# Kernel tuning notes

Hardware: AMD Instinct MI355X
Metric: run time of the kernel (lower is better)

## Reference

```python
import jax, jax.numpy as jnp
import numpy as np

B, NQ, NV = 4, 16384, 16384
DIM, FRAMES = 64, 4
D = DIM * FRAMES            # embed_dims = 256
HEADS, POINTS, LEVELS = 8, 4, 1
HD = D // HEADS             # head_dim = 32
HL, WL = 128, 128           # single-level feature map, HL*WL == NV
EPS = 1e-6


def setup_inputs() -> dict:
    key = jax.random.key(0)
    ks = jax.random.split(key, 14)
    inp = {
        "query": jax.random.normal(ks[0], (B, NQ, D), jnp.float32),
        "feat": jax.random.normal(ks[1], (B, NV, D), jnp.float32),
        "reference_points": jax.random.uniform(ks[2], (B, NQ, LEVELS, 2), jnp.float32),
        "spatial_shapes": jnp.array([[HL, WL]], jnp.int32),
        "level_start_index": jnp.array([0], jnp.int32),
        # LayerNorm params
        "qn_scale": jnp.ones((D,), jnp.float32),
        "qn_bias": jnp.zeros((D,), jnp.float32),
        "fn_scale": jnp.ones((D,), jnp.float32),
        "fn_bias": jnp.zeros((D,), jnp.float32),
        # MSDeformAttn projections
        "W_value": jax.random.normal(ks[3], (D, D), jnp.float32) / np.sqrt(D),
        "b_value": jnp.zeros((D,), jnp.float32),
        "W_off": jax.random.normal(ks[4], (D, HEADS * LEVELS * POINTS * 2), jnp.float32) * 0.01,
        "b_off": jax.random.normal(ks[5], (HEADS * LEVELS * POINTS * 2,), jnp.float32) * 0.5,
        "W_attn": jax.random.normal(ks[6], (D, HEADS * LEVELS * POINTS), jnp.float32) * 0.02,
        "b_attn": jnp.zeros((HEADS * LEVELS * POINTS,), jnp.float32),
        "W_out": jax.random.normal(ks[7], (D, D), jnp.float32) / np.sqrt(D),
        "b_out": jnp.zeros((D,), jnp.float32),
        # gamma is a learned scale (init 0 in the module; randomized here so it contributes)
        "gamma": jax.random.normal(ks[8], (D,), jnp.float32) * 0.1,
    }
    return inp


def _layer_norm(x, scale, bias):
    mu = jnp.mean(x, axis=-1, keepdims=True)
    var = jnp.mean(jnp.square(x - mu), axis=-1, keepdims=True)
    return (x - mu) * jax.lax.rsqrt(var + EPS) * scale + bias


def _bilinear_gather(v, loc, Hl, Wl):
    # v:   [B, H, N, hd] flattened level values (row-major HxW)
    # loc: [B, H, NQ, P, 2] normalized sampling locations in [0,1]
    # grid_sample semantics: align_corners=False, zero padding
    x = loc[..., 0] * Wl - 0.5
    y = loc[..., 1] * Hl - 0.5
    x0 = jnp.floor(x); y0 = jnp.floor(y)
    x1 = x0 + 1.0;     y1 = y0 + 1.0
    wx1 = x - x0; wx0 = 1.0 - wx1
    wy1 = y - y0; wy0 = 1.0 - wy1
    out = 0.0
    for xi, yi, w in ((x0, y0, wx0 * wy0), (x1, y0, wx1 * wy0),
                      (x0, y1, wx0 * wy1), (x1, y1, wx1 * wy1)):
        inb = (xi >= 0) & (xi < Wl) & (yi >= 0) & (yi < Hl)
        idx = (jnp.clip(yi, 0, Hl - 1) * Wl + jnp.clip(xi, 0, Wl - 1)).astype(jnp.int32)
        Bc, Hc, NQc, Pc = idx.shape
        g = jnp.take_along_axis(v, idx.reshape(Bc, Hc, NQc * Pc)[..., None], axis=2)
        g = g.reshape(Bc, Hc, NQc, Pc, -1)          # [B, H, NQ, P, hd]
        out = out + g * (w * inb)[..., None]
    return out


def reference(query, feat, reference_points, spatial_shapes, level_start_index,
              qn_scale, qn_bias, fn_scale, fn_bias,
              W_value, b_value, W_off, b_off, W_attn, b_attn, W_out, b_out, gamma):
    Bq, nq, _ = query.shape
    q = _layer_norm(query, qn_scale, qn_bias)
    v = _layer_norm(feat, fn_scale, fn_bias)

    # value projection -> per-head values [B, H, NV, hd]
    value = (v @ W_value + b_value).reshape(Bq, -1, HEADS, HD).transpose(0, 2, 1, 3)

    # sampling offsets [B, NQ, H, L, P, 2] and attention weights (softmax over L*P)
    off = (q @ W_off + b_off).reshape(Bq, nq, HEADS, LEVELS, POINTS, 2)
    aw = jax.nn.softmax((q @ W_attn + b_attn).reshape(Bq, nq, HEADS, LEVELS * POINTS), axis=-1)
    aw = aw.reshape(Bq, nq, HEADS, LEVELS, POINTS)

    ss = np.asarray(spatial_shapes)          # static level geometry
    lsi = np.asarray(level_start_index)
    offset_norm = ss[:, ::-1].astype(np.float32)  # (W, H) per level
    # sampling locations [B, NQ, H, L, P, 2]
    loc = reference_points[:, :, None, :, None, :] + off / offset_norm[None, None, None, :, None, :]

    acc = jnp.zeros((Bq, HEADS, nq, HD), query.dtype)
    for l in range(LEVELS):
        Hl, Wl = int(ss[l, 0]), int(ss[l, 1])
        start = int(lsi[l])
        v_l = value[:, :, start:start + Hl * Wl]                # [B, H, Hl*Wl, hd]
        loc_l = loc[:, :, :, l].transpose(0, 2, 1, 3, 4)        # [B, H, NQ, P, 2]
        sampled = _bilinear_gather(v_l, loc_l, Hl, Wl)          # [B, H, NQ, P, hd]
        aw_l = aw[:, :, :, l].transpose(0, 2, 1, 3)             # [B, H, NQ, P]
        acc = acc + jnp.einsum('bhnpd,bhnp->bhnd', sampled, aw_l)

    out = acc.transpose(0, 2, 1, 3).reshape(Bq, nq, D) @ W_out + b_out
    return query + gamma * out
```

## Files before the change

### kernel.cpp

```cpp
#include <hip/hip_runtime.h>

#define NQ 16384
#define NV 16384
#define DMODEL 256

typedef __bf16 bf16x8 __attribute__((ext_vector_type(8)));
typedef float f32x4 __attribute__((ext_vector_type(4)));

__device__ __forceinline__ unsigned short f2bf(float x) {
    union { float f; unsigned int u; } v; v.f = x;
    unsigned int r = v.u + 0x7fff + ((v.u >> 16) & 1);
    return (unsigned short)(r >> 16);
}
__device__ __forceinline__ float blo(unsigned int u) {
    union { unsigned int u; float f; } v; v.u = u << 16; return v.f;
}
__device__ __forceinline__ float bhi(unsigned int u) {
    union { unsigned int u; float f; } v; v.u = u & 0xFFFF0000u; return v.f;
}
__device__ __forceinline__ f32x4 mfma16(bf16x8 a, bf16x8 b, f32x4 c) {
    return __builtin_amdgcn_mfma_f32_16x16x32_bf16(a, b, c, 0, 0, 0);
}

__global__ __launch_bounds__(256) void k_prep(
    const float* __restrict__ Wv, const float* __restrict__ Woff,
    const float* __restrict__ Wattn, const float* __restrict__ Wout,
    const float* __restrict__ fns, const float* __restrict__ fnb,
    const float* __restrict__ qns, const float* __restrict__ qnb,
    const float* __restrict__ b_value, const float* __restrict__ b_off,
    const float* __restrict__ b_attn,
    unsigned short* __restrict__ WtV, unsigned short* __restrict__ WtC,
    unsigned short* __restrict__ WtO,
    float* __restrict__ csumV, float* __restrict__ preV,
    float* __restrict__ csumC, float* __restrict__ preC) {
    const int blk = blockIdx.x;
    if (blk < 608) {
        int t = blk * 256 + threadIdx.x;
        if (t < 65536) { int n = t >> 8, k = t & 255; WtV[t] = f2bf(fns[k] * Wv[k * 256 + n]); return; }
        t -= 65536;
        if (t < 65536) { int n = t >> 8, k = t & 255; WtO[t] = f2bf(Wout[k * 256 + n]); return; }
        t -= 65536;
        if (t < 24576) {
            int j = t >> 8, k = t & 255;
            float w = (j < 64) ? Woff[k * 64 + j] : Wattn[k * 32 + (j - 64)];
            WtC[j * 256 + k] = f2bf(qns[k] * w);
        }
        return;
    }
    if (blk < 612) {
        __shared__ float sCS[4][64], sPR[4][64];
        const int nl = threadIdx.x & 63;
        const int n = (blk - 608) * 64 + nl;
        const int kp = threadIdx.x >> 6;
        float cs = 0.f, pr = 0.f;
        for (int k = kp * 64; k < kp * 64 + 64; ++k) {
            float w = Wv[k * 256 + n];
            cs += fns[k] * w;
            pr += fnb[k] * w;
        }
        sCS[kp][nl] = cs; sPR[kp][nl] = pr;
        __syncthreads();
        if (threadIdx.x < 64) {
            int nn = (blk - 608) * 64 + threadIdx.x;
            csumV[nn] = sCS[0][threadIdx.x] + sCS[1][threadIdx.x] + sCS[2][threadIdx.x] + sCS[3][threadIdx.x];
            preV[nn] = sPR[0][threadIdx.x] + sPR[1][threadIdx.x] + sPR[2][threadIdx.x] + sPR[3][threadIdx.x]
                       + b_value[nn];
        }
        return;
    }
    {
        __shared__ float sCS[2][96], sPR[2][96];
        const int t = threadIdx.x;
        if (t < 192) {
            const int n = t % 96;
            const int kp = t / 96;
            float cs = 0.f, pr = 0.f;
            for (int k = kp * 128; k < kp * 128 + 128; ++k) {
                float w = (n < 64) ? Woff[k * 64 + n] : Wattn[k * 32 + (n - 64)];
                cs += qns[k] * w;
                pr += qnb[k] * w;
            }
            sCS[kp][n] = cs; sPR[kp][n] = pr;
        }
        __syncthreads();
        if (t < 96) {
            csumC[t] = sCS[0][t] + sCS[1][t];
            preC[t] = sPR[0][t] + sPR[1][t] + ((t < 64) ? b_off[t] : b_attn[t - 64]);
        }
        return;
    }
}

#define STAGE_LNSTATS64(srcptr)                                                       \
    {                                                                                 \
        const int t = threadIdx.x;                                                    \
        const float4* src4 = (const float4*)((srcptr) + (size_t)m0 * 256);            \
        _Pragma("unroll 4") for (int i = 0; i < 16; ++i) {                            \
            float4 x = src4[i * 256 + t];                                             \
            const int row = i * 4 + (t >> 6);                                         \
            uint2 pk;                                                                 \
            pk.x = (unsigned)f2bf(x.x) | ((unsigned)f2bf(x.y) << 16);                 \
            pk.y = (unsigned)f2bf(x.z) | ((unsigned)f2bf(x.w) << 16);                 \
            *(uint2*)&A[row * 264 + (t & 63) * 4] = pk;                               \
        }                                                                             \
    }                                                                                 \
    __syncthreads();                                                                  \
    {                                                                                 \
        const int t = threadIdx.x;                                                    \
        const int r = t >> 2, h = t & 3;                                              \
        float s = 0.f, sq = 0.f;                                                      \
        _Pragma("unroll") for (int j = 0; j < 8; ++j) {                               \
            uint4 u = *(const uint4*)&A[r * 264 + h * 64 + j * 8];                    \
            float v0 = blo(u.x), v1 = bhi(u.x), v2 = blo(u.y), v3 = bhi(u.y);         \
            float v4 = blo(u.z), v5 = bhi(u.z), v6 = blo(u.w), v7 = bhi(u.w);         \
            s += v0 + v1 + v2 + v3 + v4 + v5 + v6 + v7;                               \
            sq += v0 * v0 + v1 * v1 + v2 * v2 + v3 * v3 +                             \
                  v4 * v4 + v5 * v5 + v6 * v6 + v7 * v7;                              \
        }                                                                             \
        s += __shfl_xor(s, 1);  sq += __shfl_xor(sq, 1);                              \
        s += __shfl_xor(s, 2);  sq += __shfl_xor(sq, 2);                              \
        if (h == 0) {                                                                 \
            float mu = s * 0.00390625f;                                               \
            muL[r] = mu;                                                              \
            rsL[r] = rsqrtf(sq * 0.00390625f - mu * mu + 1e-6f);                      \
        }                                                                             \
    }

#define STAGE_A64(srcbuf)                                                             \
    {                                                                                 \
        const int c = threadIdx.x & 31;                                               \
        const int rt = threadIdx.x >> 5;                                              \
        _Pragma("unroll") for (int i = 0; i < 8; ++i) {                               \
            const int r = rt + i * 8;                                                 \
            *(uint4*)&A[r * 264 + c * 8] =                                            \
                *(const uint4*)((srcbuf) + (size_t)(m0 + r) * 256 + c * 8);           \
        }                                                                             \
    }

#define MFMA_STEP4(bf, kk)                                                            \
    _Pragma("unroll") for (int m = 0; m < 4; ++m) {                                   \
        bf16x8 a = *(const bf16x8*)&A[(m * 16 + lrow) * 264 + (kk) * 32 + lk];        \
        _Pragma("unroll") for (int i = 0; i < 4; ++i)                                 \
            acc[i][m] = mfma16(bf[i], a, acc[i][m]);                                  \
    }

__global__ __launch_bounds__(256, 4) void k_mlp(
    const float* __restrict__ feat, const float* __restrict__ csumV,
    const float* __restrict__ preV, const unsigned short* __restrict__ WtV,
    unsigned short* __restrict__ value,
    const float* __restrict__ query, const float* __restrict__ refpt,
    const float* __restrict__ csumC, const float* __restrict__ preC,
    const unsigned short* __restrict__ WtC, float4* __restrict__ samples) {
    __shared__ unsigned short A[64 * 264];
    __shared__ float muL[64], rsL[64];
    const int blk = blockIdx.x;
    const int m0 = (blk >> 1) * 64;
    const int lane = threadIdx.x & 63;
    const int w = threadIdx.x >> 6;

    if ((blk & 1) == 0) {
        STAGE_LNSTATS64(feat)
        const int lrow = lane & 15, lk = (lane >> 4) * 8;
        f32x4 acc[4][4];
#pragma unroll
        for (int i = 0; i < 4; ++i)
#pragma unroll
            for (int m = 0; m < 4; ++m) acc[i][m] = (f32x4){0.f, 0.f, 0.f, 0.f};
#define LOADB_V(dst, kk)                                                              \
    _Pragma("unroll") for (int i = 0; i < 4; ++i) dst[i] =                            \
        *(const bf16x8*)(WtV + (size_t)((w * 4 + i) * 16 + lrow) * 256 + (kk) * 32 + lk);
        {
            bf16x8 b0[4], b1[4];
            LOADB_V(b0, 0)
#pragma unroll
            for (int k2 = 0; k2 < 4; ++k2) {
                LOADB_V(b1, k2 * 2 + 1)
                MFMA_STEP4(b0, k2 * 2)
                if (k2 < 3) { LOADB_V(b0, k2 * 2 + 2) }
                MFMA_STEP4(b1, k2 * 2 + 1)
            }
        }
        __syncthreads();
        const int g = lane >> 4;
#pragma unroll
        for (int i = 0; i < 4; ++i) {
            const int col0 = (w * 4 + i) * 16 + g * 4;
            float4 cs = *(const float4*)(csumV + col0);
            float4 pr = *(const float4*)(preV + col0);
#pragma unroll
            for (int m = 0; m < 4; ++m) {
                const int rl = m * 16 + (lane & 15);
                float mu = muL[rl], rs = rsL[rl];
                uint2 r;
                r.x = (unsigned)f2bf(rs * (acc[i][m][0] - mu * cs.x) + pr.x) |
                      ((unsigned)f2bf(rs * (acc[i][m][1] - mu * cs.y) + pr.y) << 16);
                r.y = (unsigned)f2bf(rs * (acc[i][m][2] - mu * cs.z) + pr.z) |
                      ((unsigned)f2bf(rs * (acc[i][m][3] - mu * cs.w) + pr.w) << 16);
                *(uint2*)&A[rl * 264 + col0] = r;
            }
        }
        __syncthreads();
        {
            const int c = threadIdx.x & 31;
            const int rt = threadIdx.x >> 5;
#pragma unroll
            for (int i = 0; i < 8; ++i) {
                const int r = rt + i * 8;
                *(uint4*)(value + (size_t)(m0 + r) * 256 + c * 8) = *(uint4*)&A[r * 264 + c * 8];
            }
        }
    } else {
        float* DlA = (float*)A;
        const int lrow = lane & 15, g = lane >> 4, lk = g * 8;
        const float4* qrow = (const float4*)(query + (size_t)(m0 + w * 16 + lrow) * 256) + g * 2;
        f32x4 acc[6];
#pragma unroll
        for (int i = 0; i < 6; ++i) acc[i] = (f32x4){0.f, 0.f, 0.f, 0.f};
        float s = 0.f, sq = 0.f;
#pragma unroll
        for (int kk = 0; kk < 8; ++kk) {
            float4 xa = qrow[kk * 8];
            float4 xb = qrow[kk * 8 + 1];
            s  += xa.x + xa.y + xa.z + xa.w + xb.x + xb.y + xb.z + xb.w;
            sq += xa.x * xa.x + xa.y * xa.y + xa.z * xa.z + xa.w * xa.w +
                  xb.x * xb.x + xb.y * xb.y + xb.z * xb.z + xb.w * xb.w;
            union { bf16x8 v; unsigned short u[8]; } af;
            af.u[0] = f2bf(xa.x); af.u[1] = f2bf(xa.y); af.u[2] = f2bf(xa.z); af.u[3] = f2bf(xa.w);
            af.u[4] = f2bf(xb.x); af.u[5] = f2bf(xb.y); af.u[6] = f2bf(xb.z); af.u[7] = f2bf(xb.w);
            bf16x8 b[6];
#pragma unroll
            for (int i = 0; i < 6; ++i)
                b[i] = *(const bf16x8*)(WtC + (size_t)(i * 16 + lrow) * 256 + kk * 32 + lk);
#pragma unroll
            for (int i = 0; i < 6; ++i) acc[i] = mfma16(b[i], af.v, acc[i]);
        }
        s += __shfl_xor(s, 16); sq += __shfl_xor(sq, 16);
        s += __shfl_xor(s, 32); sq += __shfl_xor(sq, 32);
        if (lane < 16) {
            float mu = s * 0.00390625f;
            muL[w * 16 + lane] = mu;
            rsL[w * 16 + lane] = rsqrtf(sq * 0.00390625f - mu * mu + 1e-6f);
        }
        float* Dl = DlA + w * 1600;
#pragma unroll
        for (int i = 0; i < 6; ++i) {
            *(float4*)&Dl[lrow * 100 + i * 16 + g * 4] =
                make_float4(acc[i][0], acc[i][1], acc[i][2], acc[i][3]);
        }
        __syncthreads();
#pragma unroll
        for (int it = 0; it < 2; ++it) {
            int idx = it * 64 + lane;
            int rl = idx >> 3;
            int h = idx & 7;
            int row = m0 + w * 16 + rl;
            float mu = muL[w * 16 + rl], rs = rsL[w * 16 + rl];
            float rx = refpt[(size_t)row * 2 + 0] * 128.f - 0.5f;
            float ry = refpt[(size_t)row * 2 + 1] * 128.f - 0.5f;
            float l0 = rs * (Dl[rl * 100 + 64 + h * 4 + 0] - mu * csumC[64 + h * 4 + 0]) + preC[64 + h * 4 + 0];
            float l1 = rs * (Dl[rl * 100 + 64 + h * 4 + 1] - mu * csumC[64 + h * 4 + 1]) + preC[64 + h * 4 + 1];
            float l2 = rs * (Dl[rl * 100 + 64 + h * 4 + 2] - mu * csumC[64 + h * 4 + 2]) + preC[64 + h * 4 + 2];
            float l3 = rs * (Dl[rl * 100 + 64 + h * 4 + 3] - mu * csumC[64 + h * 4 + 3]) + preC[64 + h * 4 + 3];
            float mx = fmaxf(fmaxf(l0, l1), fmaxf(l2, l3));
            float e0 = __expf(l0 - mx), e1 = __expf(l1 - mx);
            float e2 = __expf(l2 - mx), e3 = __expf(l3 - mx);
            float inv = 1.f / (e0 + e1 + e2 + e3);
            float ww[4] = {e0 * inv, e1 * inv, e2 * inv, e3 * inv};
#pragma unroll
            for (int p = 0; p < 4; ++p) {
                float ox = rs * (Dl[rl * 100 + h * 8 + p * 2 + 0] - mu * csumC[h * 8 + p * 2 + 0]) + preC[h * 8 + p * 2 + 0];
                float oy = rs * (Dl[rl * 100 + h * 8 + p * 2 + 1] - mu * csumC[h * 8 + p * 2 + 1]) + preC[h * 8 + p * 2 + 1];
                samples[((size_t)row * 8 + h) * 4 + p] = make_float4(rx + ox, ry + oy, ww[p], 0.f);
            }
        }
    }
}

__global__ __launch_bounds__(256) void k_gather(
    const unsigned short* __restrict__ value, const float4* __restrict__ samples,
    unsigned short* __restrict__ accb) {
    const int tid = blockIdx.x * 256 + threadIdx.x;
    const int sub = tid & 3;
    const int t = tid >> 2;
    const int h = t & 7;
    const int bq = t >> 3;
    const int b = bq >> 14;
    const unsigned short* vb = value + ((size_t)b << 14) * 256 + h * 32 + sub * 8;
    float a0 = 0.f, a1 = 0.f, a2 = 0.f, a3 = 0.f;
    float a4 = 0.f, a5 = 0.f, a6 = 0.f, a7 = 0.f;
#pragma unroll
    for (int p = 0; p < 4; ++p) {
        float4 s = samples[(size_t)t * 4 + p];
        float xf = floorf(s.x), yf = floorf(s.y);
        float fx = s.x - xf, fy = s.y - yf;
        int x0 = (int)xf, y0 = (int)yf;
        int x1 = x0 + 1, y1 = y0 + 1;
        float wgt = s.z;
        bool bx0 = (unsigned)x0 < 128u, bx1 = (unsigned)x1 < 128u;
        bool by0 = (unsigned)y0 < 128u, by1 = (unsigned)y1 < 128u;
        float wt[4];
        wt[0] = (bx0 && by0) ? (1.f - fx) * (1.f - fy) * wgt : 0.f;
        wt[1] = (bx1 && by0) ? fx * (1.f - fy) * wgt : 0.f;
        wt[2] = (bx0 && by1) ? (1.f - fx) * fy * wgt : 0.f;
        wt[3] = (bx1 && by1) ? fx * fy * wgt : 0.f;
        int xc0 = min(max(x0, 0), 127), xc1 = min(max(x1, 0), 127);
        int yc0 = min(max(y0, 0), 127), yc1 = min(max(y1, 0), 127);
        int pix[4];
        pix[0] = yc0 * 128 + xc0; pix[1] = yc0 * 128 + xc1;
        pix[2] = yc1 * 128 + xc0; pix[3] = yc1 * 128 + xc1;
#pragma unroll
        for (int tp = 0; tp < 4; ++tp) {
            uint4 u = *(const uint4*)(vb + (size_t)pix[tp] * 256);
            float w = wt[tp];
            a0 = fmaf(w, blo(u.x), a0); a1 = fmaf(w, bhi(u.x), a1);
            a2 = fmaf(w, blo(u.y), a2); a3 = fmaf(w, bhi(u.y), a3);
            a4 = fmaf(w, blo(u.z), a4); a5 = fmaf(w, bhi(u.z), a5);
            a6 = fmaf(w, blo(u.w), a6); a7 = fmaf(w, bhi(u.w), a7);
        }
    }
    uint4 r;
    r.x = (unsigned)f2bf(a0) | ((unsigned)f2bf(a1) << 16);
    r.y = (unsigned)f2bf(a2) | ((unsigned)f2bf(a3) << 16);
    r.z = (unsigned)f2bf(a4) | ((unsigned)f2bf(a5) << 16);
    r.w = (unsigned)f2bf(a6) | ((unsigned)f2bf(a7) << 16);
    *(uint4*)(accb + (size_t)bq * 256 + h * 32 + sub * 8) = r;
}

__global__ __launch_bounds__(256, 4) void k_out(
    const unsigned short* __restrict__ accb, const unsigned short* __restrict__ WtO,
    const float* __restrict__ b_out, const float* __restrict__ gamma,
    const float* __restrict__ query, float* __restrict__ out) {
    __shared__ unsigned short A[64 * 264];
    const int m0 = blockIdx.x * 64;
    STAGE_A64(accb)
    __syncthreads();
    const int lane = threadIdx.x & 63;
    const int w = threadIdx.x >> 6;
    const int lrow = lane & 15, lk = (lane >> 4) * 8;
    f32x4 acc[4][4];
#pragma unroll
    for (int i = 0; i < 4; ++i)
#pragma unroll
        for (int m = 0; m < 4; ++m) acc[i][m] = (f32x4){0.f, 0.f, 0.f, 0.f};
#define LOADB_O(dst, kk)                                                              \
    _Pragma("unroll") for (int i = 0; i < 4; ++i) dst[i] =                            \
        *(const bf16x8*)(WtO + (size_t)((w * 4 + i) * 16 + lrow) * 256 + (kk) * 32 + lk);
    {
        bf16x8 b0[4], b1[4];
        LOADB_O(b0, 0)
#pragma unroll
        for (int k2 = 0; k2 < 4; ++k2) {
            LOADB_O(b1, k2 * 2 + 1)
            MFMA_STEP4(b0, k2 * 2)
            if (k2 < 3) { LOADB_O(b0, k2 * 2 + 2) }
            MFMA_STEP4(b1, k2 * 2 + 1)
        }
    }
    const int g = lane >> 4;
    float4 bo[4], gm[4];
#pragma unroll
    for (int i = 0; i < 4; ++i) {
        bo[i] = *(const float4*)(b_out + (w * 4 + i) * 16 + g * 4);
        gm[i] = *(const float4*)(gamma + (w * 4 + i) * 16 + g * 4);
    }
#pragma unroll
    for (int m = 0; m < 4; ++m) {
        const size_t row = (size_t)(m0 + m * 16 + (lane & 15));
#pragma unroll
        for (int i = 0; i < 4; ++i) {
            const int col0 = (w * 4 + i) * 16 + g * 4;
            float4 q = *(const float4*)(query + row * 256 + col0);
            float4 o;
            o.x = q.x + gm[i].x * (acc[i][m][0] + bo[i].x);
            o.y = q.y + gm[i].y * (acc[i][m][1] + bo[i].y);
            o.z = q.z + gm[i].z * (acc[i][m][2] + bo[i].z);
            o.w = q.w + gm[i].w * (acc[i][m][3] + bo[i].w);
            *(float4*)(out + row * 256 + col0) = o;
        }
    }
}

extern "C" void kernel_launch(void* const* d_in, const int* in_sizes, int n_in,
                              void* d_out, int out_size, void* d_ws, size_t ws_size,
                              hipStream_t stream) {
    const float* query    = (const float*)d_in[0];
    const float* feat     = (const float*)d_in[1];
    const float* refpt    = (const float*)d_in[2];
    const float* qn_scale = (const float*)d_in[5];
    const float* qn_bias  = (const float*)d_in[6];
    const float* fn_scale = (const float*)d_in[7];
    const float* fn_bias  = (const float*)d_in[8];
    const float* W_value  = (const float*)d_in[9];
    const float* b_value  = (const float*)d_in[10];
    const float* W_off    = (const float*)d_in[11];
    const float* b_off    = (const float*)d_in[12];
    const float* W_attn   = (const float*)d_in[13];
    const float* b_attn   = (const float*)d_in[14];
    const float* W_out    = (const float*)d_in[15];
    const float* b_out    = (const float*)d_in[16];
    const float* gamma    = (const float*)d_in[17];
    float* out = (float*)d_out;

    char* ws = (char*)d_ws;
    unsigned short* WtV   = (unsigned short*)(ws);
    unsigned short* WtO   = (unsigned short*)(ws + 131072);
    unsigned short* WtC   = (unsigned short*)(ws + 262144);
    float* csumV = (float*)(ws + 311296);
    float* preV  = (float*)(ws + 312320);
    float* csumC = (float*)(ws + 313344);
    float* preC  = (float*)(ws + 313856);
    unsigned short* value = (unsigned short*)(ws + 315392);
    float4* samples       = (float4*)(ws + 315392 + 33554432);
    unsigned short* accb  = (unsigned short*)(ws + 315392 + 2 * 33554432);

    hipLaunchKernelGGL(k_prep, dim3(613), dim3(256), 0, stream,
                       W_value, W_off, W_attn, W_out,
                       fn_scale, fn_bias, qn_scale, qn_bias,
                       b_value, b_off, b_attn,
                       WtV, WtC, WtO, csumV, preV, csumC, preC);
    hipLaunchKernelGGL(k_mlp, dim3(2048), dim3(256), 0, stream,
                       feat, csumV, preV, WtV, value,
                       query, refpt, csumC, preC, WtC, samples);
    hipLaunchKernelGGL(k_gather, dim3(8192), dim3(256), 0, stream,
                       value, samples, accb);
    hipLaunchKernelGGL(k_out, dim3(1024), dim3(256), 0, stream,
                       accb, WtO, b_out, gamma, query, out);
}
```

Before: 186.4 us.

## Fuse bilinear gather into output projection kernel and make samples point-major

The separate gather kernel is merged into the output-projection kernel, so each block gathers its 64 query rows straight into shared memory as bf16 and feeds them to the MFMA GEMM. This drops the global accb round trip and one kernel launch. The samples buffer becomes point-major so reads within each point are contiguous, and a staging loop's unroll factor goes from 4 to 8. The cost is fewer threads doing the gather (1024 blocks doing 8 rows each instead of 8192 blocks), which lowers memory-level parallelism for the latency-bound random value reads.

```diff
diff --git a/kernel.cpp b/kernel.cpp
--- a/kernel.cpp
+++ b/kernel.cpp
@@ -3,6 +3,7 @@
 #define NQ 16384
 #define NV 16384
 #define DMODEL 256
+#define SAMPN (4 * 16384 * 8)
 
 typedef __bf16 bf16x8 __attribute__((ext_vector_type(8)));
 typedef float f32x4 __attribute__((ext_vector_type(4)));
@@ -95,7 +96,7 @@
     {                                                                                 \
         const int t = threadIdx.x;                                                    \
         const float4* src4 = (const float4*)((srcptr) + (size_t)m0 * 256);            \
-        _Pragma("unroll 4") for (int i = 0; i < 16; ++i) {                            \
+        _Pragma("unroll 8") for (int i = 0; i < 16; ++i) {                            \
             float4 x = src4[i * 256 + t];                                             \
             const int row = i * 4 + (t >> 6);                                         \
             uint2 pk;                                                                 \
@@ -126,17 +127,6 @@
         }                                                                             \
     }
 
-#define STAGE_A64(srcbuf)                                                             \
-    {                                                                                 \
-        const int c = threadIdx.x & 31;                                               \
-        const int rt = threadIdx.x >> 5;                                              \
-        _Pragma("unroll") for (int i = 0; i < 8; ++i) {                               \
-            const int r = rt + i * 8;                                                 \
-            *(uint4*)&A[r * 264 + c * 8] =                                            \
-                *(const uint4*)((srcbuf) + (size_t)(m0 + r) * 256 + c * 8);           \
-        }                                                                             \
-    }
-
 #define MFMA_STEP4(bf, kk)                                                            \
     _Pragma("unroll") for (int m = 0; m < 4; ++m) {                                   \
         bf16x8 a = *(const bf16x8*)&A[(m * 16 + lrow) * 264 + (kk) * 32 + lk];        \
@@ -266,73 +256,75 @@
             float e2 = __expf(l2 - mx), e3 = __expf(l3 - mx);
             float inv = 1.f / (e0 + e1 + e2 + e3);
             float ww[4] = {e0 * inv, e1 * inv, e2 * inv, e3 * inv};
+            size_t trow = (size_t)row * 8 + h;
 #pragma unroll
             for (int p = 0; p < 4; ++p) {
                 float ox = rs * (Dl[rl * 100 + h * 8 + p * 2 + 0] - mu * csumC[h * 8 + p * 2 + 0]) + preC[h * 8 + p * 2 + 0];
                 float oy = rs * (Dl[rl * 100 + h * 8 + p * 2 + 1] - mu * csumC[h * 8 + p * 2 + 1]) + preC[h * 8 + p * 2 + 1];
-                samples[((size_t)row * 8 + h) * 4 + p] = make_float4(rx + ox, ry + oy, ww[p], 0.f);
-            }
-        }
-    }
-}
-
-__global__ __launch_bounds__(256) void k_gather(
+                samples[(size_t)p * SAMPN + trow] = make_float4(rx + ox, ry + oy, ww[p], 0.f);
+            }
+        }
+    }
+}
+
+__global__ __launch_bounds__(256, 4) void k_gatherout(
     const unsigned short* __restrict__ value, const float4* __restrict__ samples,
-    unsigned short* __restrict__ accb) {
-    const int tid = blockIdx.x * 256 + threadIdx.x;
-    const int sub = tid & 3;
-    const int t = tid >> 2;
-    const int h = t & 7;
-    const int bq = t >> 3;
-    const int b = bq >> 14;
-    const unsigned short* vb = value + ((size_t)b << 14) * 256 + h * 32 + sub * 8;
-    float a0 = 0.f, a1 = 0.f, a2 = 0.f, a3 = 0.f;
-    float a4 = 0.f, a5 = 0.f, a6 = 0.f, a7 = 0.f;
-#pragma unroll
-    for (int p = 0; p < 4; ++p) {
-        float4 s = samples[(size_t)t * 4 + p];
-        float xf = floorf(s.x), yf = floorf(s.y);
-        float fx = s.x - xf, fy = s.y - yf;
-        int x0 = (int)xf, y0 = (int)yf;
-        int x1 = x0 + 1, y1 = y0 + 1;
-        float wgt = s.z;
-        bool bx0 = (unsigned)x0 < 128u, bx1 = (unsigned)x1 < 128u;
-        bool by0 = (unsigned)y0 < 128u, by1 = (unsigned)y1 < 128u;
-        float wt[4];
-        wt[0] = (bx0 && by0) ? (1.f - fx) * (1.f - fy) * wgt : 0.f;
-        wt[1] = (bx1 && by0) ? fx * (1.f - fy) * wgt : 0.f;
-        wt[2] = (bx0 && by1) ? (1.f - fx) * fy * wgt : 0.f;
-        wt[3] = (bx1 && by1) ? fx * fy * wgt : 0.f;
-        int xc0 = min(max(x0, 0), 127), xc1 = min(max(x1, 0), 127);
-        int yc0 = min(max(y0, 0), 127), yc1 = min(max(y1, 0), 127);
-        int pix[4];
-        pix[0] = yc0 * 128 + xc0; pix[1] = yc0 * 128 + xc1;
-        pix[2] = yc1 * 128 + xc0; pix[3] = yc1 * 128 + xc1;
-#pragma unroll
-        for (int tp = 0; tp < 4; ++tp) {
-            uint4 u = *(const uint4*)(vb + (size_t)pix[tp] * 256);
-            float w = wt[tp];
-            a0 = fmaf(w, blo(u.x), a0); a1 = fmaf(w, bhi(u.x), a1);
-            a2 = fmaf(w, blo(u.y), a2); a3 = fmaf(w, bhi(u.y), a3);
-            a4 = fmaf(w, blo(u.z), a4); a5 = fmaf(w, bhi(u.z), a5);
-            a6 = fmaf(w, blo(u.w), a6); a7 = fmaf(w, bhi(u.w), a7);
-        }
-    }
-    uint4 r;
-    r.x = (unsigned)f2bf(a0) | ((unsigned)f2bf(a1) << 16);
-    r.y = (unsigned)f2bf(a2) | ((unsigned)f2bf(a3) << 16);
-    r.z = (unsigned)f2bf(a4) | ((unsigned)f2bf(a5) << 16);
-    r.w = (unsigned)f2bf(a6) | ((unsigned)f2bf(a7) << 16);
-    *(uint4*)(accb + (size_t)bq * 256 + h * 32 + sub * 8) = r;
-}
-
-__global__ __launch_bounds__(256, 4) void k_out(
-    const unsigned short* __restrict__ accb, const unsigned short* __restrict__ WtO,
-    const float* __restrict__ b_out, const float* __restrict__ gamma,
-    const float* __restrict__ query, float* __restrict__ out) {
+    const unsigned short* __restrict__ WtO, const float* __restrict__ b_out,
+    const float* __restrict__ gamma, const float* __restrict__ query,
+    float* __restrict__ out) {
     __shared__ unsigned short A[64 * 264];
     const int m0 = blockIdx.x * 64;
-    STAGE_A64(accb)
+    const int b = m0 >> 14;
+    const unsigned short* vbase = value + (((size_t)b << 14)) * 256;
+    {
+        const int t = threadIdx.x;
+        const int h = (t >> 2) & 7;
+        const int sub = t & 3;
+        const unsigned short* vb = vbase + h * 32 + sub * 8;
+#pragma unroll
+        for (int k = 0; k < 8; ++k) {
+            const int rl = k * 8 + (t >> 5);
+            const size_t trow = (size_t)(m0 + rl) * 8 + h;
+            float a0 = 0.f, a1 = 0.f, a2 = 0.f, a3 = 0.f;
+            float a4 = 0.f, a5 = 0.f, a6 = 0.f, a7 = 0.f;
+#pragma unroll
+            for (int p = 0; p < 4; ++p) {
+                float4 s = samples[(size_t)p * SAMPN + trow];
+                float xf = floorf(s.x), yf = floorf(s.y);
+                float fx = s.x - xf, fy = s.y - yf;
+                int x0 = (int)xf, y0 = (int)yf;
+                int x1 = x0 + 1, y1 = y0 + 1;
+                float wgt = s.z;
+                bool bx0 = (unsigned)x0 < 128u, bx1 = (unsigned)x1 < 128u;
+                bool by0 = (unsigned)y0 < 128u, by1 = (unsigned)y1 < 128u;
+                float wt[4];
+                wt[0] = (bx0 && by0) ? (1.f - fx) * (1.f - fy) * wgt : 0.f;
+                wt[1] = (bx1 && by0) ? fx * (1.f - fy) * wgt : 0.f;
+                wt[2] = (bx0 && by1) ? (1.f - fx) * fy * wgt : 0.f;
+                wt[3] = (bx1 && by1) ? fx * fy * wgt : 0.f;
+                int xc0 = min(max(x0, 0), 127), xc1 = min(max(x1, 0), 127);
+                int yc0 = min(max(y0, 0), 127), yc1 = min(max(y1, 0), 127);
+                int pix[4];
+                pix[0] = yc0 * 128 + xc0; pix[1] = yc0 * 128 + xc1;
+                pix[2] = yc1 * 128 + xc0; pix[3] = yc1 * 128 + xc1;
+#pragma unroll
+                for (int tp = 0; tp < 4; ++tp) {
+                    uint4 u = *(const uint4*)(vb + (size_t)pix[tp] * 256);
+                    float wq = wt[tp];
+                    a0 = fmaf(wq, blo(u.x), a0); a1 = fmaf(wq, bhi(u.x), a1);
+                    a2 = fmaf(wq, blo(u.y), a2); a3 = fmaf(wq, bhi(u.y), a3);
+                    a4 = fmaf(wq, blo(u.z), a4); a5 = fmaf(wq, bhi(u.z), a5);
+                    a6 = fmaf(wq, blo(u.w), a6); a7 = fmaf(wq, bhi(u.w), a7);
+                }
+            }
+            uint4 r;
+            r.x = (unsigned)f2bf(a0) | ((unsigned)f2bf(a1) << 16);
+            r.y = (unsigned)f2bf(a2) | ((unsigned)f2bf(a3) << 16);
+            r.z = (unsigned)f2bf(a4) | ((unsigned)f2bf(a5) << 16);
+            r.w = (unsigned)f2bf(a6) | ((unsigned)f2bf(a7) << 16);
+            *(uint4*)&A[rl * 264 + h * 32 + sub * 8] = r;
+        }
+    }
     __syncthreads();
     const int lane = threadIdx.x & 63;
     const int w = threadIdx.x >> 6;
@@ -411,7 +403,6 @@
     float* preC  = (float*)(ws + 313856);
     unsigned short* value = (unsigned short*)(ws + 315392);
     float4* samples       = (float4*)(ws + 315392 + 33554432);
-    unsigned short* accb  = (unsigned short*)(ws + 315392 + 2 * 33554432);
 
     hipLaunchKernelGGL(k_prep, dim3(613), dim3(256), 0, stream,
                        W_value, W_off, W_attn, W_out,
@@ -421,8 +412,6 @@
     hipLaunchKernelGGL(k_mlp, dim3(2048), dim3(256), 0, stream,
                        feat, csumV, preV, WtV, value,
                        query, refpt, csumC, preC, WtC, samples);
-    hipLaunchKernelGGL(k_gather, dim3(8192), dim3(256), 0, stream,
-                       value, samples, accb);
-    hipLaunchKernelGGL(k_out, dim3(1024), dim3(256), 0, stream,
-                       accb, WtO, b_out, gamma, query, out);
-}
+    hipLaunchKernelGGL(k_gatherout, dim3(1024), dim3(256), 0, stream,
+                       value, samples, WtO, b_out, gamma, query, out);
+}
```

After: 167.2 us. -10.3%, faster.
